# Kernel tuning notes

Measured on AMD Instinct MI355X. Metric: run time of the kernel, lower is better.

The kernel has to match this reference:

```python
import jax, jax.numpy as jnp
import numpy as np

MARGIN = 0.3


def setup_inputs() -> dict:
    key = jax.random.key(0)
    k1, k2 = jax.random.split(key)
    embeddings = jax.random.normal(k1, (4096, 128), dtype=jnp.float32)
    labels = jax.random.randint(k2, (4096,), 0, 256, dtype=jnp.int64)
    return {"embeddings": embeddings, "labels": labels}


def reference(embeddings, labels):
    # L2-normalize rows (same as F.normalize(p=2, dim=1), eps=1e-12)
    norm = jnp.maximum(jnp.linalg.norm(embeddings, axis=1, keepdims=True), 1e-12)
    e = embeddings / norm
    # cosine distance matrix [N, N]
    dist = 1.0 - e @ e.T

    same = labels[None, :] == labels[:, None]          # [N, N]
    n = labels.shape[0]
    eye = jnp.eye(n, dtype=bool)
    pos_mask = same & ~eye                             # positives excl. self
    neg_mask = ~same

    # dist in [0, 2]; finite sentinels keep max/min well-defined per row
    hardest_pos = jnp.max(jnp.where(pos_mask, dist, -1.0), axis=1)
    hardest_neg = jnp.min(jnp.where(neg_mask, dist, 3.0), axis=1)

    valid = jnp.any(pos_mask, axis=1) & jnp.any(neg_mask, axis=1)
    per_row = jax.nn.relu(hardest_pos - hardest_neg + MARGIN)
    loss_sum = jnp.sum(jnp.where(valid, per_row, 0.0))
    count = jnp.sum(valid)
    return loss_sum / jnp.maximum(count, 1).astype(loss_sum.dtype)
```

## Files before the change

kernel.cpp:

```cpp
#include <hip/hip_runtime.h>
#include <stdint.h>

typedef __bf16 bf16x8 __attribute__((ext_vector_type(8)));
typedef float f32x4 __attribute__((ext_vector_type(4)));

#define N_ROWS 4096
#define KD 128
#define BM 64
#define BN 64
#define NCHUNK 16
#define CHUNK 256
#define JT (CHUNK / BN)
#define NBLOCKS (64 * NCHUNK)
#define FIN_BLOCKS 64

__device__ __forceinline__ unsigned short f32_to_bf16_rne(float f) {
    union { float f; uint32_t u; } v; v.f = f;
    uint32_t u = v.u;
    return (unsigned short)((u + 0x7FFFu + ((u >> 16) & 1u)) >> 16);
}

__device__ __forceinline__ int swz(int row, int c) { return row * 16 + (c ^ (row & 15)); }
__device__ __forceinline__ int swzL(int L) { return (L & ~15) | ((L & 15) ^ ((L >> 4) & 15)); }

__global__ __launch_bounds__(256) void normalize_kernel(const float* __restrict__ E,
                                                        unsigned short* __restrict__ out,
                                                        float* __restrict__ gsum,
                                                        unsigned* __restrict__ gcnt,
                                                        unsigned* __restrict__ ticket) {
    if (blockIdx.x == 0 && threadIdx.x == 0) {
        *gsum = 0.0f; *gcnt = 0u; *ticket = 0u;
    }
    const int wave = threadIdx.x >> 6;
    const int lane = threadIdx.x & 63;
    const int row = blockIdx.x * 4 + wave;
    const float2 v = *(const float2*)&E[row * KD + lane * 2];
    float s = v.x * v.x + v.y * v.y;
#pragma unroll
    for (int m = 1; m < 64; m <<= 1) s += __shfl_xor(s, m, 64);
    float inv = 0.0f;
    if (s > 0.0f) {
        inv = rsqrtf(s);
        inv = inv * (1.5f - 0.5f * s * inv * inv);
    }
    const unsigned short a = f32_to_bf16_rne(v.x * inv);
    const unsigned short b = f32_to_bf16_rne(v.y * inv);
    ((uint32_t*)out)[row * (KD / 2) + lane] = ((uint32_t)b << 16) | a;
}

__global__ __launch_bounds__(256) void gram_kernel(const unsigned short* __restrict__ Ebits,
                                                   const int* __restrict__ labels,
                                                   float2* __restrict__ partials) {
    __shared__ uint4 As4[BM * KD / 8];
    __shared__ uint4 Bs4[BN * KD / 8];
    __shared__ int ljs[CHUNK];

    const int tid = threadIdx.x;
    const int itile = blockIdx.x & 63;
    const int chunk = blockIdx.x >> 6;
    const int ibase = itile * BM;
    const int cbase = chunk * CHUNK;

    {
        const uint4* src = (const uint4*)(Ebits + (size_t)ibase * KD);
#pragma unroll
        for (int it = 0; it < 4; ++it) {
            const int L = it * 256 + tid;
            As4[swzL(L)] = src[L];
        }
        ljs[tid] = labels[cbase + tid];
    }
    __syncthreads();

    const int wave = tid >> 6, lane = tid & 63;
    const int quad = lane >> 4, l15 = lane & 15;
    const int igb = ibase + wave * 16 + quad * 4;

    bf16x8 afrag[4];
#pragma unroll
    for (int s = 0; s < 4; ++s)
        afrag[s] = *(const bf16x8*)&As4[swz(wave * 16 + l15, s * 4 + quad)];

    int li_lab[4];
#pragma unroll
    for (int r = 0; r < 4; ++r) li_lab[r] = labels[igb + r];

    float minpos[4] = {2.0f, 2.0f, 2.0f, 2.0f};
    float maxneg[4] = {-2.0f, -2.0f, -2.0f, -2.0f};

    for (int jt = 0; jt < JT; ++jt) {
        const int jbase = cbase + jt * BN;
        __syncthreads();
        {
            const uint4* src = (const uint4*)(Ebits + (size_t)jbase * KD);
#pragma unroll
            for (int it = 0; it < 4; ++it) {
                const int L = it * 256 + tid;
                Bs4[swzL(L)] = src[L];
            }
        }
        __syncthreads();

#pragma unroll
        for (int t = 0; t < 4; ++t) {
            f32x4 acc = {0.f, 0.f, 0.f, 0.f};
#pragma unroll
            for (int s = 0; s < 4; ++s) {
                const bf16x8 bfrag = *(const bf16x8*)&Bs4[swz(t * 16 + l15, s * 4 + quad)];
                acc = __builtin_amdgcn_mfma_f32_16x16x32_bf16(afrag[s], bfrag, acc, 0, 0, 0);
            }
            const int jg = jbase + t * 16 + l15;
            const int lj = ljs[jt * BN + t * 16 + l15];
#pragma unroll
            for (int r = 0; r < 4; ++r) {
                const float d = acc[r];
                const bool same = (lj == li_lab[r]);
                const float dp = (same && (igb + r != jg)) ? d : 2.0f;
                const float dn = same ? -2.0f : d;
                minpos[r] = fminf(minpos[r], dp);
                maxneg[r] = fmaxf(maxneg[r], dn);
            }
        }
    }

#pragma unroll
    for (int m = 1; m < 16; m <<= 1) {
#pragma unroll
        for (int r = 0; r < 4; ++r) {
            minpos[r] = fminf(minpos[r], __shfl_xor(minpos[r], m, 64));
            maxneg[r] = fmaxf(maxneg[r], __shfl_xor(maxneg[r], m, 64));
        }
    }
    if (l15 == 0) {
#pragma unroll
        for (int r = 0; r < 4; ++r)
            partials[(igb + r) * NCHUNK + chunk] = make_float2(minpos[r], maxneg[r]);
    }
}

__global__ __launch_bounds__(256) void finalize_kernel(const float2* __restrict__ partials,
                                                       float* __restrict__ gsum,
                                                       unsigned* __restrict__ gcnt,
                                                       unsigned* __restrict__ ticket,
                                                       float* __restrict__ out) {
    __shared__ float ssum[4];
    __shared__ int scnt[4];
    __shared__ unsigned s_old;

    const int tid = threadIdx.x;
    const int sub = tid & 3;
    const int row = blockIdx.x * 64 + (tid >> 2);

    const float4* p4 = (const float4*)&partials[row * NCHUNK];
    const float4 a = p4[sub * 2];
    const float4 b = p4[sub * 2 + 1];
    float mp = fminf(fminf(a.x, a.z), fminf(b.x, b.z));
    float mn = fmaxf(fmaxf(a.y, a.w), fmaxf(b.y, b.w));
    mp = fminf(mp, __shfl_xor(mp, 1, 64)); mp = fminf(mp, __shfl_xor(mp, 2, 64));
    mn = fmaxf(mn, __shfl_xor(mn, 1, 64)); mn = fmaxf(mn, __shfl_xor(mn, 2, 64));

    float sum = 0.f; int cnt = 0;
    if (sub == 0 && mp < 1.5f && mn > -1.5f) {
        sum = fmaxf(0.f, mn - mp + 0.3f);
        cnt = 1;
    }
#pragma unroll
    for (int m = 1; m < 64; m <<= 1) {
        sum += __shfl_xor(sum, m, 64);
        cnt += __shfl_xor(cnt, m, 64);
    }
    const int wave = tid >> 6, lane = tid & 63;
    if (lane == 0) { ssum[wave] = sum; scnt[wave] = cnt; }
    __syncthreads();
    if (tid == 0) {
        atomicAdd(gsum, ssum[0] + ssum[1] + ssum[2] + ssum[3]);
        atomicAdd(gcnt, (unsigned)(scnt[0] + scnt[1] + scnt[2] + scnt[3]));
    }
    __syncthreads();
    if (tid == 0) s_old = atomicAdd(ticket, 1u);
    __syncthreads();
    if (s_old == (unsigned)(FIN_BLOCKS - 1) && tid == 0) {
        const float S = __hip_atomic_load(gsum, __ATOMIC_RELAXED, __HIP_MEMORY_SCOPE_AGENT);
        const unsigned C = __hip_atomic_load(gcnt, __ATOMIC_RELAXED, __HIP_MEMORY_SCOPE_AGENT);
        out[0] = S / (float)(C > 0u ? C : 1u);
    }
}

extern "C" void kernel_launch(void* const* d_in, const int* in_sizes, int n_in,
                              void* d_out, int out_size, void* d_ws, size_t ws_size,
                              hipStream_t stream) {
    const float* E = (const float*)d_in[0];
    const int* labels = (const int*)d_in[1];

    unsigned short* ebits = (unsigned short*)d_ws;
    float2* partials = (float2*)((char*)d_ws + (size_t)N_ROWS * KD * 2);
    float* gsum = (float*)(partials + N_ROWS * NCHUNK);
    unsigned* gcnt = (unsigned*)(gsum + 1);
    unsigned* ticket = gcnt + 1;
    float* out = (float*)d_out;

    normalize_kernel<<<N_ROWS / 4, 256, 0, stream>>>(E, ebits, gsum, gcnt, ticket);
    gram_kernel<<<NBLOCKS, 256, 0, stream>>>(ebits, labels, partials);
    finalize_kernel<<<FIN_BLOCKS, 256, 0, stream>>>(partials, gsum, gcnt, ticket, out);
}
```

Measured before the change: 74.46 us.

## Fuse finalize into gram kernel via per-tile tickets and load A fragments directly

```diff
diff --git a/kernel.cpp b/kernel.cpp
--- a/kernel.cpp
+++ b/kernel.cpp
@@ -12,7 +12,6 @@
 #define CHUNK 256
 #define JT (CHUNK / BN)
 #define NBLOCKS (64 * NCHUNK)
-#define FIN_BLOCKS 64
 
 __device__ __forceinline__ unsigned short f32_to_bf16_rne(float f) {
     union { float f; uint32_t u; } v; v.f = f;
@@ -25,12 +24,8 @@
 
 __global__ __launch_bounds__(256) void normalize_kernel(const float* __restrict__ E,
                                                         unsigned short* __restrict__ out,
-                                                        float* __restrict__ gsum,
-                                                        unsigned* __restrict__ gcnt,
-                                                        unsigned* __restrict__ ticket) {
-    if (blockIdx.x == 0 && threadIdx.x == 0) {
-        *gsum = 0.0f; *gcnt = 0u; *ticket = 0u;
-    }
+                                                        unsigned* __restrict__ ctrl) {
+    if (blockIdx.x == 0 && threadIdx.x < 67) ctrl[threadIdx.x] = 0u;
     const int wave = threadIdx.x >> 6;
     const int lane = threadIdx.x & 63;
     const int row = blockIdx.x * 4 + wave;
@@ -48,12 +43,19 @@
     ((uint32_t*)out)[row * (KD / 2) + lane] = ((uint32_t)b << 16) | a;
 }
 
-__global__ __launch_bounds__(256) void gram_kernel(const unsigned short* __restrict__ Ebits,
-                                                   const int* __restrict__ labels,
-                                                   float2* __restrict__ partials) {
-    __shared__ uint4 As4[BM * KD / 8];
+__global__ __launch_bounds__(256, 8) void gram_kernel(const unsigned short* __restrict__ Ebits,
+                                                      const int* __restrict__ labels,
+                                                      unsigned long long* __restrict__ partials,
+                                                      float* __restrict__ gsum,
+                                                      unsigned* __restrict__ gcnt,
+                                                      unsigned* __restrict__ gticket,
+                                                      unsigned* __restrict__ subticket,
+                                                      float* __restrict__ out) {
     __shared__ uint4 Bs4[BN * KD / 8];
     __shared__ int ljs[CHUNK];
+    __shared__ unsigned s_old, g_old;
+    __shared__ float ssum[4];
+    __shared__ int scnt[4];
 
     const int tid = threadIdx.x;
     const int itile = blockIdx.x & 63;
@@ -61,36 +63,29 @@
     const int ibase = itile * BM;
     const int cbase = chunk * CHUNK;
 
-    {
-        const uint4* src = (const uint4*)(Ebits + (size_t)ibase * KD);
-#pragma unroll
-        for (int it = 0; it < 4; ++it) {
-            const int L = it * 256 + tid;
-            As4[swzL(L)] = src[L];
-        }
-        ljs[tid] = labels[cbase + tid];
-    }
-    __syncthreads();
-
     const int wave = tid >> 6, lane = tid & 63;
     const int quad = lane >> 4, l15 = lane & 15;
     const int igb = ibase + wave * 16 + quad * 4;
 
     bf16x8 afrag[4];
-#pragma unroll
-    for (int s = 0; s < 4; ++s)
-        afrag[s] = *(const bf16x8*)&As4[swz(wave * 16 + l15, s * 4 + quad)];
-
+    {
+        const uint4* asrc = (const uint4*)Ebits;
+        const int arow = ibase + wave * 16 + l15;
+#pragma unroll
+        for (int s = 0; s < 4; ++s) afrag[s] = *(const bf16x8*)&asrc[arow * 16 + s * 4 + quad];
+    }
+    ljs[tid] = labels[cbase + tid];
     int li_lab[4];
 #pragma unroll
     for (int r = 0; r < 4; ++r) li_lab[r] = labels[igb + r];
+    __syncthreads();
 
     float minpos[4] = {2.0f, 2.0f, 2.0f, 2.0f};
     float maxneg[4] = {-2.0f, -2.0f, -2.0f, -2.0f};
 
     for (int jt = 0; jt < JT; ++jt) {
         const int jbase = cbase + jt * BN;
-        __syncthreads();
+        if (jt) __syncthreads();
         {
             const uint4* src = (const uint4*)(Ebits + (size_t)jbase * KD);
 #pragma unroll
@@ -133,56 +128,54 @@
     }
     if (l15 == 0) {
 #pragma unroll
-        for (int r = 0; r < 4; ++r)
-            partials[(igb + r) * NCHUNK + chunk] = make_float2(minpos[r], maxneg[r]);
-    }
-}
-
-__global__ __launch_bounds__(256) void finalize_kernel(const float2* __restrict__ partials,
-                                                       float* __restrict__ gsum,
-                                                       unsigned* __restrict__ gcnt,
-                                                       unsigned* __restrict__ ticket,
-                                                       float* __restrict__ out) {
-    __shared__ float ssum[4];
-    __shared__ int scnt[4];
-    __shared__ unsigned s_old;
-
-    const int tid = threadIdx.x;
-    const int sub = tid & 3;
-    const int row = blockIdx.x * 64 + (tid >> 2);
-
-    const float4* p4 = (const float4*)&partials[row * NCHUNK];
-    const float4 a = p4[sub * 2];
-    const float4 b = p4[sub * 2 + 1];
-    float mp = fminf(fminf(a.x, a.z), fminf(b.x, b.z));
-    float mn = fmaxf(fmaxf(a.y, a.w), fmaxf(b.y, b.w));
-    mp = fminf(mp, __shfl_xor(mp, 1, 64)); mp = fminf(mp, __shfl_xor(mp, 2, 64));
-    mn = fmaxf(mn, __shfl_xor(mn, 1, 64)); mn = fmaxf(mn, __shfl_xor(mn, 2, 64));
-
-    float sum = 0.f; int cnt = 0;
-    if (sub == 0 && mp < 1.5f && mn > -1.5f) {
-        sum = fmaxf(0.f, mn - mp + 0.3f);
-        cnt = 1;
-    }
-#pragma unroll
-    for (int m = 1; m < 64; m <<= 1) {
-        sum += __shfl_xor(sum, m, 64);
-        cnt += __shfl_xor(cnt, m, 64);
-    }
-    const int wave = tid >> 6, lane = tid & 63;
-    if (lane == 0) { ssum[wave] = sum; scnt[wave] = cnt; }
+        for (int r = 0; r < 4; ++r) {
+            union { float2 f; unsigned long long u; } pv;
+            pv.f = make_float2(minpos[r], maxneg[r]);
+            __hip_atomic_store(&partials[(igb + r) * NCHUNK + chunk], pv.u,
+                               __ATOMIC_RELAXED, __HIP_MEMORY_SCOPE_AGENT);
+        }
+    }
+
     __syncthreads();
-    if (tid == 0) {
-        atomicAdd(gsum, ssum[0] + ssum[1] + ssum[2] + ssum[3]);
-        atomicAdd(gcnt, (unsigned)(scnt[0] + scnt[1] + scnt[2] + scnt[3]));
-    }
+    if (tid == 0) s_old = atomicAdd(&subticket[itile], 1u);
     __syncthreads();
-    if (tid == 0) s_old = atomicAdd(ticket, 1u);
-    __syncthreads();
-    if (s_old == (unsigned)(FIN_BLOCKS - 1) && tid == 0) {
-        const float S = __hip_atomic_load(gsum, __ATOMIC_RELAXED, __HIP_MEMORY_SCOPE_AGENT);
-        const unsigned C = __hip_atomic_load(gcnt, __ATOMIC_RELAXED, __HIP_MEMORY_SCOPE_AGENT);
-        out[0] = S / (float)(C > 0u ? C : 1u);
+    if (s_old == (unsigned)(NCHUNK - 1)) {
+        const int rowl = tid >> 2, sub = tid & 3;
+        const unsigned long long* pp = &partials[(ibase + rowl) * NCHUNK + sub * 4];
+        float mp = 2.f, mn = -2.f;
+#pragma unroll
+        for (int k = 0; k < 4; ++k) {
+            union { float2 f; unsigned long long u; } pv;
+            pv.u = __hip_atomic_load(&pp[k], __ATOMIC_RELAXED, __HIP_MEMORY_SCOPE_AGENT);
+            mp = fminf(mp, pv.f.x);
+            mn = fmaxf(mn, pv.f.y);
+        }
+        mp = fminf(mp, __shfl_xor(mp, 1, 64)); mp = fminf(mp, __shfl_xor(mp, 2, 64));
+        mn = fmaxf(mn, __shfl_xor(mn, 1, 64)); mn = fmaxf(mn, __shfl_xor(mn, 2, 64));
+        float sum = 0.f; int cnt = 0;
+        if (sub == 0 && mp < 1.5f && mn > -1.5f) {
+            sum = fmaxf(0.f, mn - mp + 0.3f);
+            cnt = 1;
+        }
+#pragma unroll
+        for (int m = 1; m < 64; m <<= 1) {
+            sum += __shfl_xor(sum, m, 64);
+            cnt += __shfl_xor(cnt, m, 64);
+        }
+        if ((tid & 63) == 0) { ssum[tid >> 6] = sum; scnt[tid >> 6] = cnt; }
+        __syncthreads();
+        if (tid == 0) {
+            atomicAdd(gsum, ssum[0] + ssum[1] + ssum[2] + ssum[3]);
+            atomicAdd(gcnt, (unsigned)(scnt[0] + scnt[1] + scnt[2] + scnt[3]));
+        }
+        __syncthreads();
+        if (tid == 0) g_old = atomicAdd(gticket, 1u);
+        __syncthreads();
+        if (g_old == 63u && tid == 0) {
+            const float S = __hip_atomic_load(gsum, __ATOMIC_RELAXED, __HIP_MEMORY_SCOPE_AGENT);
+            const unsigned C = __hip_atomic_load(gcnt, __ATOMIC_RELAXED, __HIP_MEMORY_SCOPE_AGENT);
+            out[0] = S / (float)(C > 0u ? C : 1u);
+        }
     }
 }
 
@@ -193,13 +186,15 @@
     const int* labels = (const int*)d_in[1];
 
     unsigned short* ebits = (unsigned short*)d_ws;
-    float2* partials = (float2*)((char*)d_ws + (size_t)N_ROWS * KD * 2);
-    float* gsum = (float*)(partials + N_ROWS * NCHUNK);
-    unsigned* gcnt = (unsigned*)(gsum + 1);
-    unsigned* ticket = gcnt + 1;
+    unsigned long long* partials = (unsigned long long*)((char*)d_ws + (size_t)N_ROWS * KD * 2);
+    unsigned* ctrl = (unsigned*)(partials + N_ROWS * NCHUNK);
+    float* gsum = (float*)&ctrl[0];
+    unsigned* gcnt = &ctrl[1];
+    unsigned* gticket = &ctrl[2];
+    unsigned* subticket = &ctrl[3];
     float* out = (float*)d_out;
 
-    normalize_kernel<<<N_ROWS / 4, 256, 0, stream>>>(E, ebits, gsum, gcnt, ticket);
-    gram_kernel<<<NBLOCKS, 256, 0, stream>>>(ebits, labels, partials);
-    finalize_kernel<<<FIN_BLOCKS, 256, 0, stream>>>(partials, gsum, gcnt, ticket, out);
-}
+    normalize_kernel<<<N_ROWS / 4, 256, 0, stream>>>(E, ebits, ctrl);
+    gram_kernel<<<NBLOCKS, 256, 0, stream>>>(ebits, labels, partials, gsum, gcnt,
+                                             gticket, subticket, out);
+}
```

New measurement: 75.55 us. About the same (+1.5%).

## Load whole column chunk once into LDS and read A fragments directly from global

Applied to the files above, without the earlier changes.

```diff
diff --git a/kernel.cpp b/kernel.cpp
--- a/kernel.cpp
+++ b/kernel.cpp
@@ -7,10 +7,8 @@
 #define N_ROWS 4096
 #define KD 128
 #define BM 64
-#define BN 64
-#define NCHUNK 16
-#define CHUNK 256
-#define JT (CHUNK / BN)
+#define NCHUNK 32
+#define CHUNK 128
 #define NBLOCKS (64 * NCHUNK)
 #define FIN_BLOCKS 64
 
@@ -25,12 +23,8 @@
 
 __global__ __launch_bounds__(256) void normalize_kernel(const float* __restrict__ E,
                                                         unsigned short* __restrict__ out,
-                                                        float* __restrict__ gsum,
-                                                        unsigned* __restrict__ gcnt,
-                                                        unsigned* __restrict__ ticket) {
-    if (blockIdx.x == 0 && threadIdx.x == 0) {
-        *gsum = 0.0f; *gcnt = 0u; *ticket = 0u;
-    }
+                                                        unsigned* __restrict__ ctrl) {
+    if (blockIdx.x == 0 && threadIdx.x < 3) ctrl[threadIdx.x] = 0u;
     const int wave = threadIdx.x >> 6;
     const int lane = threadIdx.x & 63;
     const int row = blockIdx.x * 4 + wave;
@@ -51,8 +45,7 @@
 __global__ __launch_bounds__(256) void gram_kernel(const unsigned short* __restrict__ Ebits,
                                                    const int* __restrict__ labels,
                                                    float2* __restrict__ partials) {
-    __shared__ uint4 As4[BM * KD / 8];
-    __shared__ uint4 Bs4[BN * KD / 8];
+    __shared__ uint4 Bs4[CHUNK * (KD / 8)];
     __shared__ int ljs[CHUNK];
 
     const int tid = threadIdx.x;
@@ -61,65 +54,54 @@
     const int ibase = itile * BM;
     const int cbase = chunk * CHUNK;
 
-    {
-        const uint4* src = (const uint4*)(Ebits + (size_t)ibase * KD);
-#pragma unroll
-        for (int it = 0; it < 4; ++it) {
-            const int L = it * 256 + tid;
-            As4[swzL(L)] = src[L];
-        }
-        ljs[tid] = labels[cbase + tid];
-    }
-    __syncthreads();
-
     const int wave = tid >> 6, lane = tid & 63;
     const int quad = lane >> 4, l15 = lane & 15;
     const int igb = ibase + wave * 16 + quad * 4;
 
+    {
+        const uint4* src = (const uint4*)(Ebits + (size_t)cbase * KD);
+#pragma unroll
+        for (int it = 0; it < 8; ++it) {
+            const int L = it * 256 + tid;
+            Bs4[swzL(L)] = src[L];
+        }
+    }
+    if (tid < CHUNK) ljs[tid] = labels[cbase + tid];
+
     bf16x8 afrag[4];
+    {
+        const uint4* asrc = (const uint4*)Ebits;
+        const int arow = ibase + wave * 16 + l15;
 #pragma unroll
-    for (int s = 0; s < 4; ++s)
-        afrag[s] = *(const bf16x8*)&As4[swz(wave * 16 + l15, s * 4 + quad)];
-
+        for (int s = 0; s < 4; ++s) afrag[s] = *(const bf16x8*)&asrc[arow * 16 + s * 4 + quad];
+    }
     int li_lab[4];
 #pragma unroll
     for (int r = 0; r < 4; ++r) li_lab[r] = labels[igb + r];
 
+    __syncthreads();
+
     float minpos[4] = {2.0f, 2.0f, 2.0f, 2.0f};
     float maxneg[4] = {-2.0f, -2.0f, -2.0f, -2.0f};
 
-    for (int jt = 0; jt < JT; ++jt) {
-        const int jbase = cbase + jt * BN;
-        __syncthreads();
-        {
-            const uint4* src = (const uint4*)(Ebits + (size_t)jbase * KD);
 #pragma unroll
-            for (int it = 0; it < 4; ++it) {
-                const int L = it * 256 + tid;
-                Bs4[swzL(L)] = src[L];
-            }
+    for (int t = 0; t < 8; ++t) {
+        f32x4 acc = {0.f, 0.f, 0.f, 0.f};
+#pragma unroll
+        for (int s = 0; s < 4; ++s) {
+            const bf16x8 bfrag = *(const bf16x8*)&Bs4[swz(t * 16 + l15, s * 4 + quad)];
+            acc = __builtin_amdgcn_mfma_f32_16x16x32_bf16(afrag[s], bfrag, acc, 0, 0, 0);
         }
-        __syncthreads();
-
+        const int jg = cbase + t * 16 + l15;
+        const int lj = ljs[t * 16 + l15];
 #pragma unroll
-        for (int t = 0; t < 4; ++t) {
-            f32x4 acc = {0.f, 0.f, 0.f, 0.f};
-#pragma unroll
-            for (int s = 0; s < 4; ++s) {
-                const bf16x8 bfrag = *(const bf16x8*)&Bs4[swz(t * 16 + l15, s * 4 + quad)];
-                acc = __builtin_amdgcn_mfma_f32_16x16x32_bf16(afrag[s], bfrag, acc, 0, 0, 0);
-            }
-            const int jg = jbase + t * 16 + l15;
-            const int lj = ljs[jt * BN + t * 16 + l15];
-#pragma unroll
-            for (int r = 0; r < 4; ++r) {
-                const float d = acc[r];
-                const bool same = (lj == li_lab[r]);
-                const float dp = (same && (igb + r != jg)) ? d : 2.0f;
-                const float dn = same ? -2.0f : d;
-                minpos[r] = fminf(minpos[r], dp);
-                maxneg[r] = fmaxf(maxneg[r], dn);
-            }
+        for (int r = 0; r < 4; ++r) {
+            const float d = acc[r];
+            const bool same = (lj == li_lab[r]);
+            const float dp = (same && (igb + r != jg)) ? d : 2.0f;
+            const float dn = same ? -2.0f : d;
+            minpos[r] = fminf(minpos[r], dp);
+            maxneg[r] = fmaxf(maxneg[r], dn);
         }
     }
 
@@ -152,10 +134,13 @@
     const int row = blockIdx.x * 64 + (tid >> 2);
 
     const float4* p4 = (const float4*)&partials[row * NCHUNK];
-    const float4 a = p4[sub * 2];
-    const float4 b = p4[sub * 2 + 1];
-    float mp = fminf(fminf(a.x, a.z), fminf(b.x, b.z));
-    float mn = fmaxf(fmaxf(a.y, a.w), fmaxf(b.y, b.w));
+    float mp = 2.f, mn = -2.f;
+#pragma unroll
+    for (int k = 0; k < 4; ++k) {
+        const float4 v = p4[sub * 4 + k];
+        mp = fminf(mp, fminf(v.x, v.z));
+        mn = fmaxf(mn, fmaxf(v.y, v.w));
+    }
     mp = fminf(mp, __shfl_xor(mp, 1, 64)); mp = fminf(mp, __shfl_xor(mp, 2, 64));
     mn = fmaxf(mn, __shfl_xor(mn, 1, 64)); mn = fmaxf(mn, __shfl_xor(mn, 2, 64));
 
@@ -194,12 +179,13 @@
 
     unsigned short* ebits = (unsigned short*)d_ws;
     float2* partials = (float2*)((char*)d_ws + (size_t)N_ROWS * KD * 2);
-    float* gsum = (float*)(partials + N_ROWS * NCHUNK);
-    unsigned* gcnt = (unsigned*)(gsum + 1);
-    unsigned* ticket = gcnt + 1;
+    unsigned* ctrl = (unsigned*)(partials + N_ROWS * NCHUNK);
+    float* gsum = (float*)&ctrl[0];
+    unsigned* gcnt = &ctrl[1];
+    unsigned* ticket = &ctrl[2];
     float* out = (float*)d_out;
 
-    normalize_kernel<<<N_ROWS / 4, 256, 0, stream>>>(E, ebits, gsum, gcnt, ticket);
+    normalize_kernel<<<N_ROWS / 4, 256, 0, stream>>>(E, ebits, ctrl);
     gram_kernel<<<NBLOCKS, 256, 0, stream>>>(ebits, labels, partials);
     finalize_kernel<<<FIN_BLOCKS, 256, 0, stream>>>(partials, gsum, gcnt, ticket, out);
 }
```

New measurement: 72.98 us, median of 2. 1.02x faster.
